# Performance work log

Hardware: AMD Instinct MI355X
Metric: run time of the kernel (lower is better)

The kernel has to match this reference:

```python
import jax, jax.numpy as jnp
import numpy as np

HIDDEN = 3072
HEADS = 24
HEAD_DIM = HIDDEN // HEADS  # 128
MLP_HIDDEN = 4 * HIDDEN     # 12288
IMG_LEN = 1024
TXT_LEN = 256
L = IMG_LEN + TXT_LEN
B = 1
EPS = 1e-6


def setup_inputs() -> dict:
    key = jax.random.key(0)
    ks = jax.random.split(key, 12)
    x = jax.random.normal(ks[0], (B, L, HIDDEN), jnp.float32)
    vec = jax.random.normal(ks[1], (B, HIDDEN), jnp.float32)
    # RoPE tables: real cos/sin of position * inv_freq, repeated over pairs (full head_dim)
    inv_freq = 1.0 / (10000.0 ** (np.arange(0, HEAD_DIM, 2, dtype=np.float32) / HEAD_DIM))
    theta = np.arange(IMG_LEN, dtype=np.float32)[:, None] * inv_freq[None, :]  # [img_len, D/2]
    theta = np.repeat(theta, 2, axis=-1)  # [img_len, D]
    freqs_cos = jnp.asarray(np.cos(theta))[None, :, None, :]  # [1, img_len, 1, D]
    freqs_sin = jnp.asarray(np.sin(theta))[None, :, None, :]
    s = 0.02
    mod_w = jax.random.normal(ks[2], (HIDDEN, 3 * HIDDEN), jnp.float32) * s
    mod_b = jnp.zeros((3 * HIDDEN,), jnp.float32)
    w1 = jax.random.normal(ks[3], (HIDDEN, 3 * HIDDEN + MLP_HIDDEN), jnp.float32) * s
    b1 = jnp.zeros((3 * HIDDEN + MLP_HIDDEN,), jnp.float32)
    w2 = jax.random.normal(ks[4], (HIDDEN + MLP_HIDDEN, HIDDEN), jnp.float32) * s
    b2 = jnp.zeros((HIDDEN,), jnp.float32)
    qn_w = jnp.ones((HEAD_DIM,), jnp.float32)
    kn_w = jnp.ones((HEAD_DIM,), jnp.float32)
    cu_seqlens_q = jnp.array([0, IMG_LEN, L], jnp.int32)
    cu_seqlens_kv = jnp.array([0, IMG_LEN, L], jnp.int32)
    return {"x": x, "vec": vec, "freqs_cos": freqs_cos, "freqs_sin": freqs_sin,
            "mod_w": mod_w, "mod_b": mod_b, "w1": w1, "b1": b1, "w2": w2, "b2": b2,
            "qn_w": qn_w, "kn_w": kn_w, "img_len": IMG_LEN,
            "cu_seqlens_q": cu_seqlens_q, "cu_seqlens_kv": cu_seqlens_kv}


def _layernorm(x):  # elementwise_affine=False
    mu = jnp.mean(x, axis=-1, keepdims=True)
    var = jnp.mean(jnp.square(x - mu), axis=-1, keepdims=True)
    return (x - mu) * jax.lax.rsqrt(var + EPS)


def _rmsnorm(x, w):
    ms = jnp.mean(jnp.square(x), axis=-1, keepdims=True)
    return x * jax.lax.rsqrt(ms + EPS) * w


def _rope_interleaved(x, cos, sin):
    # mode=1: rotate interleaved pairs: (-x1, x0, -x3, x2, ...)
    x0 = x[..., 0::2]
    x1 = x[..., 1::2]
    rot = jnp.stack([-x1, x0], axis=-1).reshape(x.shape)
    return x * cos + rot * sin


def reference(x, vec, freqs_cos, freqs_sin, mod_w, mod_b, w1, b1, w2, b2,
              qn_w, kn_w, img_len, cu_seqlens_q, cu_seqlens_kv):
    bs = x.shape[0]
    assert cu_seqlens_q.shape[0] == 2 * bs + 1
    # adaLN modulation: SiLU -> Linear(hidden, 3*hidden)
    mod = jax.nn.silu(vec) @ mod_w + mod_b           # [B, 3H]
    mod = mod[:, None, :]                             # [B, 1, 3H]
    mod_shift, mod_scale, mod_gate = jnp.split(mod, 3, axis=-1)
    x_mod = _layernorm(x) * (1.0 + mod_scale) + mod_shift
    # fused QKV + MLP projection
    h = x_mod @ w1 + b1                               # [B, L, 3*hidden + mlp]
    qkv = h[..., :3 * HIDDEN]
    mlp = h[..., 3 * HIDDEN:]
    # 'B L (K H D) -> K B L H D'
    qkv = qkv.reshape(bs, -1, 3, HEADS, HEAD_DIM)
    q, k, v = qkv[:, :, 0], qkv[:, :, 1], qkv[:, :, 2]  # [B, L, H, D]
    q = _rmsnorm(q, qn_w)
    k = _rmsnorm(k, kn_w)
    # RoPE on image tokens only
    img_q = _rope_interleaved(q[:, :img_len], freqs_cos, freqs_sin)
    img_k = _rope_interleaved(k[:, :img_len], freqs_cos, freqs_sin)
    q = jnp.concatenate([img_q, q[:, img_len:]], axis=1)
    k = jnp.concatenate([img_k, k[:, img_len:]], axis=1)
    # dense attention (bs==1 path, no mask), scale = 1/sqrt(head_dim)
    scale = 1.0 / jnp.sqrt(jnp.float32(HEAD_DIM))
    scores = jnp.einsum('bqhd,bkhd->bhqk', q, k) * scale
    probs = jax.nn.softmax(scores, axis=-1)
    attn = jnp.einsum('bhqk,bkhd->bqhd', probs, v)
    attn = attn.reshape(bs, -1, HEADS * HEAD_DIM)     # [B, L, hidden]
    # output projection on concat(attn, gelu_tanh(mlp))
    out = jnp.concatenate([attn, jax.nn.gelu(mlp, approximate=True)], axis=-1) @ w2 + b2
    return x + out * mod_gate
```

## Files before the change

kernel.cpp:

```cpp
#include <hip/hip_runtime.h>
#include <cstdint>
#include <cstddef>

typedef __bf16 bf16x8_t __attribute__((ext_vector_type(8)));
typedef float f32x4 __attribute__((ext_vector_type(4)));

#define HID 3072
#define NHEADS 24
#define HD 128
#define MLP 12288
#define SEQ 1280
#define IMG 1024
#define N1 21504
#define QKVW 9216
#define A2W 15360
#define EPSV 1e-6f

__device__ __forceinline__ size_t tpos(int row, int col, int KT) {
    return ((size_t)(row >> 8) * KT + (col >> 6)) * 16384
         + (size_t)(((((col >> 5) & 1) << 4) + ((row >> 4) & 15)) * 512
                    + (((row & 15) + (((col >> 3) & 3) << 4)) << 3) + (col & 7));
}

__device__ __forceinline__ void gload16(const void* g, void* l) {
    __builtin_amdgcn_global_load_lds(
        (const __attribute__((address_space(1))) unsigned int*)g,
        (__attribute__((address_space(3))) unsigned int*)l, 16, 0, 0);
}

__device__ __forceinline__ void bar() {
    asm volatile("" ::: "memory");
    __builtin_amdgcn_s_barrier();
    asm volatile("" ::: "memory");
}

__device__ __forceinline__ void conv_tile(const float* __restrict__ in, ushort* __restrict__ out,
                                          int N, int KT, int kb, int nb, int tid,
                                          float (*tle)[65]) {
    int k0 = kb * 64, n0 = nb * 64;
    int rr = tid >> 2, cg = (tid & 3) * 16;
    #pragma unroll
    for (int j = 0; j < 4; ++j) {
        float4 vv = *reinterpret_cast<const float4*>(&in[(size_t)(k0 + rr) * N + n0 + cg + j * 4]);
        tle[rr][cg + j * 4 + 0] = vv.x;
        tle[rr][cg + j * 4 + 1] = vv.y;
        tle[rr][cg + j * 4 + 2] = vv.z;
        tle[rr][cg + j * 4 + 3] = vv.w;
    }
    __syncthreads();
    int nl = tid & 63;
    #pragma unroll
    for (int gg = 0; gg < 2; ++gg) {
        int g = (tid >> 6) + gg * 4;
        union { ushort u[8]; uint4 q; } pk;
        #pragma unroll
        for (int j = 0; j < 8; ++j)
            pk.u[j] = __builtin_bit_cast(ushort, (__bf16)tle[g * 8 + j][nl]);
        *reinterpret_cast<uint4*>(&out[tpos(n0 + nl, k0 + g * 8, KT)]) = pk.q;
    }
}

__global__ void silu_kernel(const float* __restrict__ v, float* __restrict__ sv) {
    int i = blockIdx.x * 256 + threadIdx.x;
    float x = v[i];
    sv[i] = x / (1.f + expf(-x));
}

__global__ __launch_bounds__(256) void gemvconv_fat(const float* __restrict__ sv,
                                                    const float* __restrict__ W,
                                                    float* __restrict__ part,
                                                    const float* __restrict__ w1,
                                                    ushort* __restrict__ w1b) {
    __shared__ float tle[64][65];
    int bid = blockIdx.x;
    int tid = threadIdx.x;
    if (bid < 288) {
        int n = (bid % 36) * 256 + tid;
        int k0 = (bid / 36) * 384;
        float s = 0.f;
        for (int k = k0; k < k0 + 384; ++k)
            s = fmaf(sv[k], W[(size_t)k * QKVW + n], s);
        part[(size_t)(bid / 36) * QKVW + n] = s;
        return;
    }
    int cb = bid - 288;
    conv_tile(w1, w1b, N1, HID / 64, cb % 48, cb / 48, tid, tle);
}

__global__ void gemv_reduce(const float* __restrict__ part, const float* __restrict__ bias,
                            float* __restrict__ mod) {
    int n = blockIdx.x * 256 + threadIdx.x;
    float s = bias[n];
    #pragma unroll
    for (int ky = 0; ky < 8; ++ky) s += part[(size_t)ky * QKVW + n];
    mod[n] = s;
}

__global__ __launch_bounds__(384) void ln_mod_kernel(const float* __restrict__ x,
                                                     const float* __restrict__ mod,
                                                     ushort* __restrict__ xmt) {
    int m = blockIdx.x;
    int t = threadIdx.x;
    int lane = t & 63, w = t >> 6;
    const float* xr = x + (size_t)m * HID;
    float4 v0 = *reinterpret_cast<const float4*>(&xr[t * 8]);
    float4 v1 = *reinterpret_cast<const float4*>(&xr[t * 8 + 4]);
    float s = v0.x + v0.y + v0.z + v0.w + v1.x + v1.y + v1.z + v1.w;
    float sq = v0.x * v0.x + v0.y * v0.y + v0.z * v0.z + v0.w * v0.w +
               v1.x * v1.x + v1.y * v1.y + v1.z * v1.z + v1.w * v1.w;
    #pragma unroll
    for (int off = 1; off < 64; off <<= 1) {
        s += __shfl_xor(s, off);
        sq += __shfl_xor(sq, off);
    }
    __shared__ float red[12];
    if (lane == 0) { red[w] = s; red[w + 6] = sq; }
    __syncthreads();
    s = red[0] + red[1] + red[2] + red[3] + red[4] + red[5];
    sq = red[6] + red[7] + red[8] + red[9] + red[10] + red[11];
    float mu = s * (1.f / HID);
    float var = sq * (1.f / HID) - mu * mu;
    float rs = rsqrtf(var + EPSV);
    float vals[8] = {v0.x, v0.y, v0.z, v0.w, v1.x, v1.y, v1.z, v1.w};
    union { ushort u[8]; uint4 q; } pk;
    #pragma unroll
    for (int j = 0; j < 8; ++j) {
        int n = t * 8 + j;
        float y = (vals[j] - mu) * rs * (1.f + mod[HID + n]) + mod[n];
        pk.u[j] = __builtin_bit_cast(ushort, (__bf16)y);
    }
    *reinterpret_cast<uint4*>(&xmt[tpos(m, t * 8, HID >> 6)]) = pk.q;
}

template <int EPI, int SPLITS>
__global__ __launch_bounds__(512, 2) void gemm8p(
    const ushort* __restrict__ At, const ushort* __restrict__ Bt,
    const float* __restrict__ bias, float* __restrict__ outf, ushort* __restrict__ outb,
    int KTtot, int NTloc, int NTN) {
    int nwg = gridDim.x;
    int q = nwg >> 3, r = nwg & 7;
    int orig = blockIdx.x;
    int xcd = orig & 7;
    int wgid = (xcd < r ? xcd * (q + 1) : r * (q + 1) + (xcd - r) * q) + (orig >> 3);
    int mt = wgid % 5;
    int p = wgid / 5;
    int nt = p % NTN;
    int sp = p / NTN;
    int kOff = sp * NTloc;
    int m0 = mt * 256, n0 = nt * 256;

    __shared__ ushort LA[2][16384];
    __shared__ ushort LB[2][16384];

    int tid = threadIdx.x;
    int lane = tid & 63, wid = tid >> 6;
    int wm = wid >> 2, wn = wid & 3;
    int lr = lane & 15, lg = lane >> 4;

    const ushort* gA = At + (size_t)mt * KTtot * 16384;
    const ushort* gB = Bt + (size_t)nt * KTtot * 16384;

    f32x4 acc[8][4] = {};
    bf16x8_t af0[4][2], af1[4][2], bf0[2][2], bf1[2][2];

    auto stage = [&](ushort (*L)[16384], int buf, const ushort* g, int ktG) {
        #pragma unroll
        for (int j = 0; j < 4; ++j) {
            int b = wid * 4 + j;
            gload16(g + (size_t)ktG * 16384 + b * 512 + lane * 8, &L[buf][b * 512]);
        }
    };
    auto rdA = [&](int buf, int h, bf16x8_t (&af)[4][2]) {
        #pragma unroll
        for (int mi = 0; mi < 4; ++mi)
            #pragma unroll
            for (int k = 0; k < 2; ++k)
                af[mi][k] = *reinterpret_cast<const bf16x8_t*>(
                    &LA[buf][(k * 16 + wm * 8 + h * 4 + mi) * 512 + lane * 8]);
    };
    auto rdB = [&](int buf, int v, bf16x8_t (&bf)[2][2]) {
        #pragma unroll
        for (int ni = 0; ni < 2; ++ni)
            #pragma unroll
            for (int k = 0; k < 2; ++k)
                bf[ni][k] = *reinterpret_cast<const bf16x8_t*>(
                    &LB[buf][(k * 16 + wn * 4 + v * 2 + ni) * 512 + lane * 8]);
    };
    auto mmq = [&](bf16x8_t (&af)[4][2], bf16x8_t (&bf)[2][2], int h, int v) {
        __builtin_amdgcn_s_setprio(1);
        #pragma unroll
        for (int mi = 0; mi < 4; ++mi)
            #pragma unroll
            for (int ni = 0; ni < 2; ++ni)
                #pragma unroll
                for (int k = 0; k < 2; ++k)
                    acc[h * 4 + mi][v * 2 + ni] = __builtin_amdgcn_mfma_f32_16x16x32_bf16(
                        af[mi][k], bf[ni][k], acc[h * 4 + mi][v * 2 + ni], 0, 0, 0);
        __builtin_amdgcn_s_setprio(0);
    };

    stage(LA, 0, gA, kOff);
    stage(LB, 0, gB, kOff);
    stage(LA, 1, gA, kOff + 1);
    stage(LB, 1, gB, kOff + 1);
    asm volatile("s_waitcnt vmcnt(8)" ::: "memory");
    bar();
    rdA(0, 0, af0);
    rdB(0, 0, bf0);

    for (int t = 0; t < NTloc; ++t) {
        int c = t & 1;
        rdB(c, 1, bf1);
        mmq(af0, bf0, 0, 0);
        bar();
        rdA(c, 1, af1);
        mmq(af0, bf1, 0, 1);
        bar();
        if (t + 2 < NTloc) stage(LA, c, gA, kOff + t + 2);
        mmq(af1, bf0, 1, 0);
        if (t + 1 < NTloc) {
            if (t + 2 < NTloc) asm volatile("s_waitcnt vmcnt(4)" ::: "memory");
            else               asm volatile("s_waitcnt vmcnt(0)" ::: "memory");
        }
        bar();
        if (t + 1 < NTloc) {
            rdA(c ^ 1, 0, af0);
            rdB(c ^ 1, 0, bf0);
        }
        if (t + 2 < NTloc) stage(LB, c, gB, kOff + t + 2);
        mmq(af1, bf1, 1, 1);
        bar();
    }

    #pragma unroll
    for (int mi8 = 0; mi8 < 8; ++mi8) {
        #pragma unroll
        for (int nj = 0; nj < 4; ++nj) {
            int col = n0 + wn * 64 + nj * 16 + lr;
            #pragma unroll
            for (int rr2 = 0; rr2 < 4; ++rr2) {
                int row = m0 + wm * 128 + mi8 * 16 + lg * 4 + rr2;
                float val = acc[mi8][nj][rr2];
                if (EPI == 1) {
                    val += bias[col];
                    if (n0 < QKVW) {
                        outf[(size_t)row * QKVW + col] = val;
                    } else {
                        float u = 0.7978845608028654f * (val + 0.044715f * val * val * val);
                        float g = val / (1.f + __expf(-2.f * u));
                        outb[tpos(row, HID + (col - QKVW), A2W >> 6)] =
                            __builtin_bit_cast(ushort, (__bf16)g);
                    }
                } else {
                    outf[(size_t)(sp * SEQ + row) * HID + col] = val;
                }
            }
        }
    }
}

__global__ __launch_bounds__(256) void ksplit_reduce(const float* __restrict__ part,
                                                     const float* __restrict__ x,
                                                     const float* __restrict__ bias,
                                                     const float* __restrict__ gate,
                                                     float* __restrict__ out) {
    int i = blockIdx.x * 256 + threadIdx.x;
    int col = (i % (HID / 4)) * 4;
    f32x4 a = *reinterpret_cast<const f32x4*>(&part[(size_t)i * 4]);
    #pragma unroll
    for (int s = 1; s < 4; ++s) {
        f32x4 p = *reinterpret_cast<const f32x4*>(&part[(size_t)s * SEQ * HID + (size_t)i * 4]);
        #pragma unroll
        for (int c = 0; c < 4; ++c) a[c] += p[c];
    }
    f32x4 xv = *reinterpret_cast<const f32x4*>(&x[(size_t)i * 4]);
    f32x4 bv = *reinterpret_cast<const f32x4*>(&bias[col]);
    f32x4 gv = *reinterpret_cast<const f32x4*>(&gate[col]);
    f32x4 o;
    #pragma unroll
    for (int c = 0; c < 4; ++c) o[c] = xv[c] + (a[c] + bv[c]) * gv[c];
    *reinterpret_cast<f32x4*>(&out[(size_t)i * 4]) = o;
}

__global__ __launch_bounds__(256) void qkv_post(const float* __restrict__ h,
                                                const float* __restrict__ fc,
                                                const float* __restrict__ fs,
                                                const float* __restrict__ qn,
                                                const float* __restrict__ kn,
                                                __bf16* __restrict__ qb,
                                                __bf16* __restrict__ kb,
                                                __bf16* __restrict__ vb) {
    int m = blockIdx.x;
    int lane = threadIdx.x & 63, w = threadIdx.x >> 6;
    for (int rr = w; rr < 72; rr += 4) {
        int s = rr / 24, hd = rr % 24;
        const float* src = h + (size_t)m * QKVW + s * HID + hd * HD;
        float2 xv = *reinterpret_cast<const float2*>(&src[2 * lane]);
        float x0 = xv.x, x1 = xv.y;
        if (s < 2) {
            float ss = x0 * x0 + x1 * x1;
            #pragma unroll
            for (int off = 1; off < 64; off <<= 1) ss += __shfl_xor(ss, off);
            float rs = rsqrtf(ss * (1.f / HD) + EPSV);
            const float* nw = (s == 0) ? qn : kn;
            x0 *= rs * nw[2 * lane];
            x1 *= rs * nw[2 * lane + 1];
            if (m < IMG) {
                float c0 = fc[m * HD + 2 * lane], c1 = fc[m * HD + 2 * lane + 1];
                float s0 = fs[m * HD + 2 * lane], s1 = fs[m * HD + 2 * lane + 1];
                float r0 = x0 * c0 - x1 * s0;
                float r1 = x1 * c1 + x0 * s1;
                x0 = r0; x1 = r1;
            }
        }
        __bf16* dst = ((s == 0) ? qb : (s == 1) ? kb : vb) + (size_t)hd * SEQ * HD + (size_t)m * HD + 2 * lane;
        ushort u0 = __builtin_bit_cast(ushort, (__bf16)x0);
        ushort u1 = __builtin_bit_cast(ushort, (__bf16)x1);
        *reinterpret_cast<uint*>(dst) = (uint)u0 | ((uint)u1 << 16);
    }
}

__global__ __launch_bounds__(256) void attn_fat(const __bf16* __restrict__ qb,
                                                const __bf16* __restrict__ kb,
                                                const __bf16* __restrict__ vb,
                                                ushort* __restrict__ a2,
                                                const float* __restrict__ w2,
                                                ushort* __restrict__ w2b) {
    __shared__ float tle[64][65];
    int bid = blockIdx.x;
    int tid = threadIdx.x;
    if (bid >= 480) {
        int cb = bid - 480;
        conv_tile(w2, w2b, HID, A2W / 64, cb % 240, cb / 240, tid, tle);
        return;
    }
    __shared__ alignas(16) __bf16 Kl[32][136];
    __shared__ alignas(16) __bf16 Vl[32][136];
    __shared__ float Pl[4][32][16];

    int head = bid / 20;
    int lane = tid & 63, w = tid >> 6;
    int lr = lane & 15, lg = lane >> 4;
    int q0 = (bid % 20) * 64 + w * 16;
    const __bf16* Q = qb + (size_t)head * SEQ * HD;
    const __bf16* Kp = kb + (size_t)head * SEQ * HD;
    const __bf16* Vp = vb + (size_t)head * SEQ * HD;

    bf16x8_t qf[4];
    #pragma unroll
    for (int kc = 0; kc < 4; ++kc)
        qf[kc] = *reinterpret_cast<const bf16x8_t*>(&Q[(size_t)(q0 + lr) * HD + kc * 32 + lg * 8]);

    float m_run = -1e30f, l_run = 0.f;
    f32x4 of[8] = {};
    const float sm_scale = 0.08838834764831845f;

    for (int kv0 = 0; kv0 < SEQ; kv0 += 32) {
        #pragma unroll
        for (int cc = 0; cc < 2; ++cc) {
            int c = tid + cc * 256;
            int row = c >> 4, off = (c & 15) * 8;
            *reinterpret_cast<bf16x8_t*>(&Kl[row][off]) =
                *reinterpret_cast<const bf16x8_t*>(&Kp[(size_t)(kv0 + row) * HD + off]);
            *reinterpret_cast<bf16x8_t*>(&Vl[row][off]) =
                *reinterpret_cast<const bf16x8_t*>(&Vp[(size_t)(kv0 + row) * HD + off]);
        }
        __syncthreads();

        f32x4 st[2] = {};
        #pragma unroll
        for (int h = 0; h < 2; ++h)
            #pragma unroll
            for (int kc = 0; kc < 4; ++kc) {
                bf16x8_t kf = *reinterpret_cast<const bf16x8_t*>(&Kl[h * 16 + lr][kc * 32 + lg * 8]);
                st[h] = __builtin_amdgcn_mfma_f32_16x16x32_bf16(kf, qf[kc], st[h], 0, 0, 0);
            }
        float sarr[8];
        #pragma unroll
        for (int h = 0; h < 2; ++h)
            #pragma unroll
            for (int r = 0; r < 4; ++r) sarr[h * 4 + r] = st[h][r] * sm_scale;

        float mloc = sarr[0];
        #pragma unroll
        for (int i = 1; i < 8; ++i) mloc = fmaxf(mloc, sarr[i]);
        mloc = fmaxf(mloc, __shfl_xor(mloc, 16));
        mloc = fmaxf(mloc, __shfl_xor(mloc, 32));
        float m_new = fmaxf(m_run, mloc);
        float alpha = expf(m_run - m_new);
        float pv[8], psum = 0.f;
        #pragma unroll
        for (int i = 0; i < 8; ++i) { pv[i] = expf(sarr[i] - m_new); psum += pv[i]; }
        psum += __shfl_xor(psum, 16);
        psum += __shfl_xor(psum, 32);
        l_run = l_run * alpha + psum;
        m_run = m_new;

        #pragma unroll
        for (int h = 0; h < 2; ++h)
            #pragma unroll
            for (int r = 0; r < 4; ++r) Pl[w][h * 16 + lg * 4 + r][lr] = pv[h * 4 + r];
        bf16x8_t pa;
        #pragma unroll
        for (int j = 0; j < 8; ++j) pa[j] = (__bf16)Pl[w][lg * 8 + j][lr];

        float alr[4];
        #pragma unroll
        for (int r = 0; r < 4; ++r) alr[r] = __shfl(alpha, lg * 4 + r);

        #pragma unroll
        for (int db = 0; db < 8; ++db) {
            #pragma unroll
            for (int r = 0; r < 4; ++r) of[db][r] *= alr[r];
            bf16x8_t vv;
            #pragma unroll
            for (int j = 0; j < 8; ++j) vv[j] = Vl[lg * 8 + j][db * 16 + lr];
            of[db] = __builtin_amdgcn_mfma_f32_16x16x32_bf16(pa, vv, of[db], 0, 0, 0);
        }
        __syncthreads();
    }

    float lr4[4];
    #pragma unroll
    for (int r = 0; r < 4; ++r) lr4[r] = __shfl(l_run, lg * 4 + r);
    #pragma unroll
    for (int db = 0; db < 8; ++db)
        #pragma unroll
        for (int r = 0; r < 4; ++r) {
            int row = q0 + lg * 4 + r;
            int col = head * HD + db * 16 + lr;
            a2[tpos(row, col, A2W >> 6)] =
                __builtin_bit_cast(ushort, (__bf16)(of[db][r] / lr4[r]));
        }
}

extern "C" void kernel_launch(void* const* d_in, const int* in_sizes, int n_in,
                              void* d_out, int out_size, void* d_ws, size_t ws_size,
                              hipStream_t stream) {
    const float* x = (const float*)d_in[0];
    const float* vec = (const float*)d_in[1];
    const float* fc = (const float*)d_in[2];
    const float* fs = (const float*)d_in[3];
    const float* mod_w = (const float*)d_in[4];
    const float* mod_b = (const float*)d_in[5];
    const float* w1 = (const float*)d_in[6];
    const float* b1 = (const float*)d_in[7];
    const float* w2 = (const float*)d_in[8];
    const float* b2 = (const float*)d_in[9];
    const float* qn = (const float*)d_in[10];
    const float* kn = (const float*)d_in[11];
    float* out = (float*)d_out;

    char* ws = (char*)d_ws;
    size_t off = 0;
    float* sv = (float*)(ws + off); off += 3072 * 4;
    float* mod = (float*)(ws + off); off += 9216 * 4;
    float* part = (float*)(ws + off); off += 8 * 9216 * 4;
    off = (off + 255) & ~(size_t)255;
    ushort* xmt = (ushort*)(ws + off); off += (size_t)SEQ * HID * 2;
    off = (off + 255) & ~(size_t)255;
    float* hqkv = (float*)(ws + off); off += (size_t)SEQ * QKVW * 4;
    __bf16* qb = (__bf16*)(ws + off); off += (size_t)NHEADS * SEQ * HD * 2;
    __bf16* kb = (__bf16*)(ws + off); off += (size_t)NHEADS * SEQ * HD * 2;
    __bf16* vb = (__bf16*)(ws + off); off += (size_t)NHEADS * SEQ * HD * 2;
    off = (off + 255) & ~(size_t)255;
    ushort* a2t = (ushort*)(ws + off); off += (size_t)SEQ * A2W * 2;
    float* part2 = hqkv;

    off = (off + 255) & ~(size_t)255;
    ushort* w1b = (ushort*)(ws + off);
    ushort* w2b = w1b;

    silu_kernel<<<12, 256, 0, stream>>>(vec, sv);
    gemvconv_fat<<<288 + 48 * 336, 256, 0, stream>>>(sv, mod_w, part, w1, w1b);
    gemv_reduce<<<36, 256, 0, stream>>>(part, mod_b, mod);
    ln_mod_kernel<<<SEQ, 384, 0, stream>>>(x, mod, xmt);

    gemm8p<1, 1><<<5 * (N1 / 256), 512, 0, stream>>>(xmt, w1b, b1, hqkv, a2t,
                                                     HID / 64, HID / 64, N1 / 256);
    qkv_post<<<SEQ, 256, 0, stream>>>(hqkv, fc, fs, qn, kn, qb, kb, vb);
    attn_fat<<<480 + 240 * 48, 256, 0, stream>>>(qb, kb, vb, a2t, w2, w2b);
    gemm8p<2, 4><<<4 * 5 * (HID / 256), 512, 0, stream>>>(a2t, w2b, nullptr, part2, nullptr,
                                                          A2W / 64, A2W / 64 / 4, HID / 256);
    ksplit_reduce<<<SEQ * HID / 1024, 256, 0, stream>>>(part2, x, b2, mod + 2 * HID, out);
}
```

Baseline: 628.1 us.

## Restructure GEMM into 4-stage K32 pipeline and store intermediates as bf16

The GEMM kernel now stages 32-wide K slices into a 4-deep LDS ring, with a single fragment load and a full 8x4 MFMA block per step, replacing the 2-stage 64-wide interleaved schedule. The QKV output and the split-K partials are also written as bf16 instead of fp32, and qkv_post and ksplit_reduce are changed to read bf16. This is meant to hide global-load latency better and to halve intermediate memory traffic. In exchange it adds more barriers per K step, and rounding the split-K partials to bf16 before summing loses precision.

```diff
diff --git a/kernel.cpp b/kernel.cpp
--- a/kernel.cpp
+++ b/kernel.cpp
@@ -34,6 +34,13 @@
     asm volatile("" ::: "memory");
 }
 
+__device__ __forceinline__ float bf2f(uint u) {
+    return __builtin_bit_cast(float, u << 16);
+}
+__device__ __forceinline__ ushort f2bfu(float f) {
+    return __builtin_bit_cast(ushort, (__bf16)f);
+}
+
 __device__ __forceinline__ void conv_tile(const float* __restrict__ in, ushort* __restrict__ out,
                                           int N, int KT, int kb, int nb, int tid,
                                           float (*tle)[65]) {
@@ -55,7 +62,7 @@
         union { ushort u[8]; uint4 q; } pk;
         #pragma unroll
         for (int j = 0; j < 8; ++j)
-            pk.u[j] = __builtin_bit_cast(ushort, (__bf16)tle[g * 8 + j][nl]);
+            pk.u[j] = f2bfu(tle[g * 8 + j][nl]);
         *reinterpret_cast<uint4*>(&out[tpos(n0 + nl, k0 + g * 8, KT)]) = pk.q;
     }
 }
@@ -127,16 +134,16 @@
     for (int j = 0; j < 8; ++j) {
         int n = t * 8 + j;
         float y = (vals[j] - mu) * rs * (1.f + mod[HID + n]) + mod[n];
-        pk.u[j] = __builtin_bit_cast(ushort, (__bf16)y);
+        pk.u[j] = f2bfu(y);
     }
     *reinterpret_cast<uint4*>(&xmt[tpos(m, t * 8, HID >> 6)]) = pk.q;
 }
 
 template <int EPI, int SPLITS>
-__global__ __launch_bounds__(512, 2) void gemm8p(
+__global__ __launch_bounds__(512, 2) void gemmk(
     const ushort* __restrict__ At, const ushort* __restrict__ Bt,
-    const float* __restrict__ bias, float* __restrict__ outf, ushort* __restrict__ outb,
-    int KTtot, int NTloc, int NTN) {
+    const float* __restrict__ bias, ushort* __restrict__ out1, ushort* __restrict__ out2,
+    int KT64, int NT32, int NTN) {
     int nwg = gridDim.x;
     int q = nwg >> 3, r = nwg & 7;
     int orig = blockIdx.x;
@@ -146,143 +153,121 @@
     int p = wgid / 5;
     int nt = p % NTN;
     int sp = p / NTN;
-    int kOff = sp * NTloc;
+    int kOff = sp * NT32;
     int m0 = mt * 256, n0 = nt * 256;
 
-    __shared__ ushort LA[2][16384];
-    __shared__ ushort LB[2][16384];
+    __shared__ ushort LA[4][8192];
+    __shared__ ushort LB[4][8192];
 
     int tid = threadIdx.x;
     int lane = tid & 63, wid = tid >> 6;
     int wm = wid >> 2, wn = wid & 3;
     int lr = lane & 15, lg = lane >> 4;
 
-    const ushort* gA = At + (size_t)mt * KTtot * 16384;
-    const ushort* gB = Bt + (size_t)nt * KTtot * 16384;
+    const ushort* gA = At + (size_t)mt * KT64 * 16384;
+    const ushort* gB = Bt + (size_t)nt * KT64 * 16384;
 
     f32x4 acc[8][4] = {};
-    bf16x8_t af0[4][2], af1[4][2], bf0[2][2], bf1[2][2];
-
-    auto stage = [&](ushort (*L)[16384], int buf, const ushort* g, int ktG) {
-        #pragma unroll
-        for (int j = 0; j < 4; ++j) {
-            int b = wid * 4 + j;
-            gload16(g + (size_t)ktG * 16384 + b * 512 + lane * 8, &L[buf][b * 512]);
+    bf16x8_t af[8], bf[4];
+
+    auto stage = [&](int sl, int tt) {
+        size_t base = (size_t)(tt >> 1) * 16384 + (size_t)(tt & 1) * 8192;
+        #pragma unroll
+        for (int j = 0; j < 2; ++j) {
+            int b = wid * 2 + j;
+            gload16(gA + base + b * 512 + lane * 8, &LA[sl][b * 512]);
+            gload16(gB + base + b * 512 + lane * 8, &LB[sl][b * 512]);
         }
     };
-    auto rdA = [&](int buf, int h, bf16x8_t (&af)[4][2]) {
-        #pragma unroll
-        for (int mi = 0; mi < 4; ++mi)
-            #pragma unroll
-            for (int k = 0; k < 2; ++k)
-                af[mi][k] = *reinterpret_cast<const bf16x8_t*>(
-                    &LA[buf][(k * 16 + wm * 8 + h * 4 + mi) * 512 + lane * 8]);
-    };
-    auto rdB = [&](int buf, int v, bf16x8_t (&bf)[2][2]) {
-        #pragma unroll
-        for (int ni = 0; ni < 2; ++ni)
-            #pragma unroll
-            for (int k = 0; k < 2; ++k)
-                bf[ni][k] = *reinterpret_cast<const bf16x8_t*>(
-                    &LB[buf][(k * 16 + wn * 4 + v * 2 + ni) * 512 + lane * 8]);
-    };
-    auto mmq = [&](bf16x8_t (&af)[4][2], bf16x8_t (&bf)[2][2], int h, int v) {
+
+    stage(0, kOff); stage(1, kOff + 1); stage(2, kOff + 2); stage(3, kOff + 3);
+    asm volatile("s_waitcnt vmcnt(12)" ::: "memory");
+    bar();
+
+    for (int t = 0; t < NT32; ++t) {
+        int sl = t & 3;
+        #pragma unroll
+        for (int mi = 0; mi < 8; ++mi)
+            af[mi] = *reinterpret_cast<const bf16x8_t*>(&LA[sl][(wm * 8 + mi) * 512 + lane * 8]);
+        #pragma unroll
+        for (int nj = 0; nj < 4; ++nj)
+            bf[nj] = *reinterpret_cast<const bf16x8_t*>(&LB[sl][(wn * 4 + nj) * 512 + lane * 8]);
         __builtin_amdgcn_s_setprio(1);
         #pragma unroll
-        for (int mi = 0; mi < 4; ++mi)
-            #pragma unroll
-            for (int ni = 0; ni < 2; ++ni)
-                #pragma unroll
-                for (int k = 0; k < 2; ++k)
-                    acc[h * 4 + mi][v * 2 + ni] = __builtin_amdgcn_mfma_f32_16x16x32_bf16(
-                        af[mi][k], bf[ni][k], acc[h * 4 + mi][v * 2 + ni], 0, 0, 0);
+        for (int mi = 0; mi < 8; ++mi)
+            #pragma unroll
+            for (int nj = 0; nj < 4; ++nj)
+                acc[mi][nj] = __builtin_amdgcn_mfma_f32_16x16x32_bf16(af[mi], bf[nj], acc[mi][nj], 0, 0, 0);
         __builtin_amdgcn_s_setprio(0);
-    };
-
-    stage(LA, 0, gA, kOff);
-    stage(LB, 0, gB, kOff);
-    stage(LA, 1, gA, kOff + 1);
-    stage(LB, 1, gB, kOff + 1);
-    asm volatile("s_waitcnt vmcnt(8)" ::: "memory");
-    bar();
-    rdA(0, 0, af0);
-    rdB(0, 0, bf0);
-
-    for (int t = 0; t < NTloc; ++t) {
-        int c = t & 1;
-        rdB(c, 1, bf1);
-        mmq(af0, bf0, 0, 0);
         bar();
-        rdA(c, 1, af1);
-        mmq(af0, bf1, 0, 1);
+        if (t + 4 < NT32) {
+            stage(sl, kOff + t + 4);
+            asm volatile("s_waitcnt vmcnt(12)" ::: "memory");
+        } else if (t + 3 < NT32) {
+            asm volatile("s_waitcnt vmcnt(8)" ::: "memory");
+        } else if (t + 2 < NT32) {
+            asm volatile("s_waitcnt vmcnt(4)" ::: "memory");
+        } else if (t + 1 < NT32) {
+            asm volatile("s_waitcnt vmcnt(0)" ::: "memory");
+        }
         bar();
-        if (t + 2 < NTloc) stage(LA, c, gA, kOff + t + 2);
-        mmq(af1, bf0, 1, 0);
-        if (t + 1 < NTloc) {
-            if (t + 2 < NTloc) asm volatile("s_waitcnt vmcnt(4)" ::: "memory");
-            else               asm volatile("s_waitcnt vmcnt(0)" ::: "memory");
-        }
-        bar();
-        if (t + 1 < NTloc) {
-            rdA(c ^ 1, 0, af0);
-            rdB(c ^ 1, 0, bf0);
-        }
-        if (t + 2 < NTloc) stage(LB, c, gB, kOff + t + 2);
-        mmq(af1, bf1, 1, 1);
-        bar();
-    }
-
-    #pragma unroll
-    for (int mi8 = 0; mi8 < 8; ++mi8) {
+    }
+
+    #pragma unroll
+    for (int mi = 0; mi < 8; ++mi) {
         #pragma unroll
         for (int nj = 0; nj < 4; ++nj) {
             int col = n0 + wn * 64 + nj * 16 + lr;
             #pragma unroll
             for (int rr2 = 0; rr2 < 4; ++rr2) {
-                int row = m0 + wm * 128 + mi8 * 16 + lg * 4 + rr2;
-                float val = acc[mi8][nj][rr2];
+                int row = m0 + wm * 128 + mi * 16 + lg * 4 + rr2;
+                float val = acc[mi][nj][rr2];
                 if (EPI == 1) {
                     val += bias[col];
                     if (n0 < QKVW) {
-                        outf[(size_t)row * QKVW + col] = val;
+                        out1[(size_t)row * QKVW + col] = f2bfu(val);
                     } else {
                         float u = 0.7978845608028654f * (val + 0.044715f * val * val * val);
                         float g = val / (1.f + __expf(-2.f * u));
-                        outb[tpos(row, HID + (col - QKVW), A2W >> 6)] =
-                            __builtin_bit_cast(ushort, (__bf16)g);
+                        out2[tpos(row, HID + (col - QKVW), A2W >> 6)] = f2bfu(g);
                     }
                 } else {
-                    outf[(size_t)(sp * SEQ + row) * HID + col] = val;
+                    out1[(size_t)(sp * SEQ + row) * HID + col] = f2bfu(val);
                 }
             }
         }
     }
 }
 
-__global__ __launch_bounds__(256) void ksplit_reduce(const float* __restrict__ part,
+__global__ __launch_bounds__(256) void ksplit_reduce(const ushort* __restrict__ partb,
                                                      const float* __restrict__ x,
                                                      const float* __restrict__ bias,
                                                      const float* __restrict__ gate,
                                                      float* __restrict__ out) {
-    int i = blockIdx.x * 256 + threadIdx.x;
-    int col = (i % (HID / 4)) * 4;
-    f32x4 a = *reinterpret_cast<const f32x4*>(&part[(size_t)i * 4]);
-    #pragma unroll
-    for (int s = 1; s < 4; ++s) {
-        f32x4 p = *reinterpret_cast<const f32x4*>(&part[(size_t)s * SEQ * HID + (size_t)i * 4]);
-        #pragma unroll
-        for (int c = 0; c < 4; ++c) a[c] += p[c];
-    }
-    f32x4 xv = *reinterpret_cast<const f32x4*>(&x[(size_t)i * 4]);
-    f32x4 bv = *reinterpret_cast<const f32x4*>(&bias[col]);
-    f32x4 gv = *reinterpret_cast<const f32x4*>(&gate[col]);
-    f32x4 o;
-    #pragma unroll
-    for (int c = 0; c < 4; ++c) o[c] = xv[c] + (a[c] + bv[c]) * gv[c];
-    *reinterpret_cast<f32x4*>(&out[(size_t)i * 4]) = o;
-}
-
-__global__ __launch_bounds__(256) void qkv_post(const float* __restrict__ h,
+    size_t i = (size_t)blockIdx.x * 256 + threadIdx.x;
+    int col = (int)((i * 8) % HID);
+    float a[8] = {};
+    #pragma unroll
+    for (int s = 0; s < 4; ++s) {
+        uint4 pv = *reinterpret_cast<const uint4*>(&partb[(size_t)s * SEQ * HID + i * 8]);
+        uint w[4] = {pv.x, pv.y, pv.z, pv.w};
+        #pragma unroll
+        for (int c = 0; c < 4; ++c) {
+            a[c * 2]     += bf2f(w[c] & 0xffffu);
+            a[c * 2 + 1] += __builtin_bit_cast(float, w[c] & 0xffff0000u);
+        }
+    }
+    f32x4 o0, o1;
+    #pragma unroll
+    for (int j = 0; j < 4; ++j) {
+        o0[j] = x[i * 8 + j] + (a[j] + bias[col + j]) * gate[col + j];
+        o1[j] = x[i * 8 + 4 + j] + (a[4 + j] + bias[col + 4 + j]) * gate[col + 4 + j];
+    }
+    *reinterpret_cast<f32x4*>(&out[i * 8]) = o0;
+    *reinterpret_cast<f32x4*>(&out[i * 8 + 4]) = o1;
+}
+
+__global__ __launch_bounds__(256) void qkv_post(const ushort* __restrict__ hb,
                                                 const float* __restrict__ fc,
                                                 const float* __restrict__ fs,
                                                 const float* __restrict__ qn,
@@ -294,9 +279,10 @@
     int lane = threadIdx.x & 63, w = threadIdx.x >> 6;
     for (int rr = w; rr < 72; rr += 4) {
         int s = rr / 24, hd = rr % 24;
-        const float* src = h + (size_t)m * QKVW + s * HID + hd * HD;
-        float2 xv = *reinterpret_cast<const float2*>(&src[2 * lane]);
-        float x0 = xv.x, x1 = xv.y;
+        const ushort* src = hb + (size_t)m * QKVW + s * HID + hd * HD;
+        uint pair = *reinterpret_cast<const uint*>(&src[2 * lane]);
+        float x0 = bf2f(pair & 0xffffu);
+        float x1 = __builtin_bit_cast(float, pair & 0xffff0000u);
         if (s < 2) {
             float ss = x0 * x0 + x1 * x1;
             #pragma unroll
@@ -314,9 +300,8 @@
             }
         }
         __bf16* dst = ((s == 0) ? qb : (s == 1) ? kb : vb) + (size_t)hd * SEQ * HD + (size_t)m * HD + 2 * lane;
-        ushort u0 = __builtin_bit_cast(ushort, (__bf16)x0);
-        ushort u1 = __builtin_bit_cast(ushort, (__bf16)x1);
-        *reinterpret_cast<uint*>(dst) = (uint)u0 | ((uint)u1 << 16);
+        uint u0 = f2bfu(x0), u1 = f2bfu(x1);
+        *reinterpret_cast<uint*>(dst) = u0 | (u1 << 16);
     }
 }
 
@@ -429,8 +414,7 @@
         for (int r = 0; r < 4; ++r) {
             int row = q0 + lg * 4 + r;
             int col = head * HD + db * 16 + lr;
-            a2[tpos(row, col, A2W >> 6)] =
-                __builtin_bit_cast(ushort, (__bf16)(of[db][r] / lr4[r]));
+            a2[tpos(row, col, A2W >> 6)] = f2bfu(of[db][r] / lr4[r]);
         }
 }
 
@@ -459,13 +443,13 @@
     off = (off + 255) & ~(size_t)255;
     ushort* xmt = (ushort*)(ws + off); off += (size_t)SEQ * HID * 2;
     off = (off + 255) & ~(size_t)255;
-    float* hqkv = (float*)(ws + off); off += (size_t)SEQ * QKVW * 4;
+    ushort* hqkvb = (ushort*)(ws + off); off += (size_t)SEQ * QKVW * 2;
     __bf16* qb = (__bf16*)(ws + off); off += (size_t)NHEADS * SEQ * HD * 2;
     __bf16* kb = (__bf16*)(ws + off); off += (size_t)NHEADS * SEQ * HD * 2;
     __bf16* vb = (__bf16*)(ws + off); off += (size_t)NHEADS * SEQ * HD * 2;
     off = (off + 255) & ~(size_t)255;
     ushort* a2t = (ushort*)(ws + off); off += (size_t)SEQ * A2W * 2;
-    float* part2 = hqkv;
+    ushort* partb = hqkvb;
 
     off = (off + 255) & ~(size_t)255;
     ushort* w1b = (ushort*)(ws + off);
@@ -476,11 +460,11 @@
     gemv_reduce<<<36, 256, 0, stream>>>(part, mod_b, mod);
     ln_mod_kernel<<<SEQ, 384, 0, stream>>>(x, mod, xmt);
 
-    gemm8p<1, 1><<<5 * (N1 / 256), 512, 0, stream>>>(xmt, w1b, b1, hqkv, a2t,
-                                                     HID / 64, HID / 64, N1 / 256);
-    qkv_post<<<SEQ, 256, 0, stream>>>(hqkv, fc, fs, qn, kn, qb, kb, vb);
+    gemmk<1, 1><<<5 * (N1 / 256), 512, 0, stream>>>(xmt, w1b, b1, hqkvb, a2t,
+                                                    HID / 64, HID / 32, N1 / 256);
+    qkv_post<<<SEQ, 256, 0, stream>>>(hqkvb, fc, fs, qn, kn, qb, kb, vb);
     attn_fat<<<480 + 240 * 48, 256, 0, stream>>>(qb, kb, vb, a2t, w2, w2b);
-    gemm8p<2, 4><<<4 * 5 * (HID / 256), 512, 0, stream>>>(a2t, w2b, nullptr, part2, nullptr,
-                                                          A2W / 64, A2W / 64 / 4, HID / 256);
-    ksplit_reduce<<<SEQ * HID / 1024, 256, 0, stream>>>(part2, x, b2, mod + 2 * HID, out);
-}
+    gemmk<2, 4><<<4 * 5 * (HID / 256), 512, 0, stream>>>(a2t, w2b, nullptr, partb, nullptr,
+                                                         A2W / 64, A2W / 32 / 4, HID / 256);
+    ksplit_reduce<<<SEQ * HID / 2048, 256, 0, stream>>>(partb, x, b2, mod + 2 * HID, out);
+}
```

Result: slower. 731.9 us (+16.5%).
